# Kernel tuning notes

Measured on AMD Instinct MI355X. Metric: run time of the kernel, lower is better.

The kernel has to match this reference:

```python
import jax, jax.numpy as jnp
import numpy as np

N_IN, N_OUT, K, G = 128, 256, 3, 3  # G = grid intervals (setup hard-codes 3)
KNOT_LO, KNOT_HI = -1.0, 1.0


def make_grid(n, k, G, lo=KNOT_LO, hi=KNOT_HI):
    # Augmented knot vector: G+1 knots extended by k on each side -> G+2k+1 points
    h = (hi - lo) / G
    g = jnp.arange(-k, G + k + 1, dtype=jnp.float32) * h + lo
    return jnp.tile(g[None, :], (n, 1))  # (n, G+2k+1)


def get_spline_basis(x, grid, k):
    # Cox-de Boor recursion. x: (batch, n); grid: (n, G+2k+1)
    g = grid[None, :, :]          # (1, n, G+2k+1)
    xx = x[:, :, None]            # (batch, n, 1)
    # order-0 (indicator) basis: (batch, n, G+2k)
    basis = ((xx >= g[..., :-1]) & (xx < g[..., 1:])).astype(x.dtype)
    for kk in range(1, k + 1):
        left = (xx - g[..., : -(kk + 1)]) / (g[..., kk:-1] - g[..., : -(kk + 1)]) * basis[..., :-1]
        right = (g[..., kk + 1 :] - xx) / (g[..., kk + 1 :] - g[..., 1:-kk]) * basis[..., 1:]
        basis = left + right
    return basis  # (batch, n, G+k)


def setup_inputs() -> dict:
    key = jax.random.key(0)
    k1, k2 = jax.random.split(key)
    batch = 512
    n = N_IN * N_OUT
    x = jax.random.normal(k1, (batch, N_IN), dtype=jnp.float32)
    grid = make_grid(n, K, G)                                        # state (non-trainable)
    c_basis = 0.1 * jax.random.normal(k2, (n, G + K), dtype=jnp.float32)
    c_spl = jnp.ones((n,), dtype=jnp.float32)
    c_res = jnp.ones((n,), dtype=jnp.float32)
    return {"x": x, "grid": grid, "c_basis": c_basis, "c_spl": c_spl, "c_res": c_res}


def reference(x, grid, c_basis, c_spl, c_res):
    batch = x.shape[0]
    # Broadcast each input node to every output edge, out-major ordering:
    # einsum('ij,k->ikj', x, ones(n_out)).reshape(batch, n_in*n_out)
    x_ext = jnp.broadcast_to(x[:, None, :], (batch, N_OUT, N_IN)).reshape(batch, N_OUT * N_IN)
    # residual branch: swish, transposed to (n, batch)
    res = jax.nn.swish(x_ext).T
    # spline branch: (batch, n, G+K) basis combined with per-edge coeffs -> (n, batch)
    Bi = get_spline_basis(x_ext, grid, K)
    spl = jnp.einsum('ij,bij->ib', c_basis, Bi)
    y = c_spl[:, None] * spl + c_res[:, None] * res            # (n, batch)
    y = y.reshape(N_OUT, N_IN, batch).sum(axis=1) / N_IN       # (n_out, batch)
    return y.T                                                 # (batch, n_out)
```

## Files before the change

kernel.cpp:

```cpp
#include <hip/hip_runtime.h>
#include <hip/hip_bf16.h>


typedef short short8 __attribute__((ext_vector_type(8)));
typedef float f32x4 __attribute__((ext_vector_type(4)));

static __device__ inline unsigned short bf16_bits(float f) {
    union { __hip_bfloat16 h; unsigned short u; } cvt;
    cvt.h = __float2bfloat16(f);
    return cvt.u;
}

__global__ __launch_bounds__(256) void build_fw(
    const float* __restrict__ x,
    const float* __restrict__ grid,
    const float* __restrict__ c_basis,
    const float* __restrict__ c_spl,
    const float* __restrict__ c_res,
    unsigned short* __restrict__ F,
    unsigned short* __restrict__ W)
{
    const int tid = blockIdx.x * 256 + threadIdx.x;

    if (tid < 512 * 128) {
        float t[10];
#pragma unroll
        for (int m = 0; m < 10; ++m) t[m] = grid[m];

        const float xv = x[tid];

        float b0[9];
#pragma unroll
        for (int s = 0; s < 9; ++s)
            b0[s] = (xv >= t[s] && xv < t[s + 1]) ? 1.0f : 0.0f;
        float b1[8];
#pragma unroll
        for (int s = 0; s < 8; ++s)
            b1[s] = (xv - t[s]) / (t[s + 1] - t[s]) * b0[s]
                  + (t[s + 2] - xv) / (t[s + 2] - t[s + 1]) * b0[s + 1];
        float b2[7];
#pragma unroll
        for (int s = 0; s < 7; ++s)
            b2[s] = (xv - t[s]) / (t[s + 2] - t[s]) * b1[s]
                  + (t[s + 3] - xv) / (t[s + 3] - t[s + 1]) * b1[s + 1];
        float b3[6];
#pragma unroll
        for (int s = 0; s < 6; ++s)
            b3[s] = (xv - t[s]) / (t[s + 3] - t[s]) * b2[s]
                  + (t[s + 4] - xv) / (t[s + 4] - t[s + 1]) * b2[s + 1];

        const float sw = xv / (1.0f + expf(-xv));

        unsigned short* dst = F + tid * 7;
#pragma unroll
        for (int s = 0; s < 6; ++s) dst[s] = bf16_bits(b3[s]);
        dst[6] = bf16_bits(sw);
    } else if (tid < 512 * 128 + 32768) {
        const int j = tid - 512 * 128;
        unsigned short* dst = W + j * 7;
        const float spl = c_spl[j];
#pragma unroll
        for (int s = 0; s < 6; ++s) dst[s] = bf16_bits(spl * c_basis[j * 6 + s]);
        dst[6] = bf16_bits(c_res[j]);
    }
}

__global__ __launch_bounds__(64) void kan_gemm(
    const unsigned short* __restrict__ F,
    const unsigned short* __restrict__ W,
    float* __restrict__ out)
{
    const int bt   = blockIdx.x >> 4;
    const int ot   = blockIdx.x & 15;
    const int lane = threadIdx.x;
    const int r    = lane & 15;
    const int q    = lane >> 4;

    const unsigned short* fp = F + (bt * 16 + r) * 896 + q * 8;
    const unsigned short* wp = W + (ot * 16 + r) * 896 + q * 8;

    f32x4 acc = {0.0f, 0.0f, 0.0f, 0.0f};

#pragma unroll
    for (int k0 = 0; k0 < 896; k0 += 128) {
        short8 a0 = *(const short8*)(fp + k0);
        short8 a1 = *(const short8*)(fp + k0 + 32);
        short8 a2 = *(const short8*)(fp + k0 + 64);
        short8 a3 = *(const short8*)(fp + k0 + 96);
        short8 w0 = *(const short8*)(wp + k0);
        short8 w1 = *(const short8*)(wp + k0 + 32);
        short8 w2 = *(const short8*)(wp + k0 + 64);
        short8 w3 = *(const short8*)(wp + k0 + 96);
        acc = __builtin_amdgcn_mfma_f32_16x16x32_bf16(a0, w0, acc, 0, 0, 0);
        acc = __builtin_amdgcn_mfma_f32_16x16x32_bf16(a1, w1, acc, 0, 0, 0);
        acc = __builtin_amdgcn_mfma_f32_16x16x32_bf16(a2, w2, acc, 0, 0, 0);
        acc = __builtin_amdgcn_mfma_f32_16x16x32_bf16(a3, w3, acc, 0, 0, 0);
    }

    const float scale = 1.0f / 128.0f;
    const int orow = bt * 16 + q * 4;
    const int ocol = ot * 16 + r;
#pragma unroll
    for (int reg = 0; reg < 4; ++reg)
        out[(orow + reg) * 256 + ocol] = acc[reg] * scale;
}

extern "C" void kernel_launch(void* const* d_in, const int* in_sizes, int n_in,
                              void* d_out, int out_size, void* d_ws, size_t ws_size,
                              hipStream_t stream) {
    const float* x       = (const float*)d_in[0];
    const float* grid    = (const float*)d_in[1];
    const float* c_basis = (const float*)d_in[2];
    const float* c_spl   = (const float*)d_in[3];
    const float* c_res   = (const float*)d_in[4];
    float* out = (float*)d_out;

    unsigned short* F = (unsigned short*)d_ws;
    unsigned short* W = (unsigned short*)((char*)d_ws + 512 * 896 * 2);

    build_fw<<<384, 256, 0, stream>>>(x, grid, c_basis, c_spl, c_res, F, W);
    kan_gemm<<<512, 64, 0, stream>>>(F, W, out);
}
```

Before: 68.50 us.

## Fuse basis/weight construction and MFMA GEMM into one LDS-staged kernel

```diff
diff --git a/kernel.cpp b/kernel.cpp
--- a/kernel.cpp
+++ b/kernel.cpp
@@ -1,9 +1,13 @@
 #include <hip/hip_runtime.h>
 #include <hip/hip_bf16.h>
+#include <math.h>
 
 
 typedef short short8 __attribute__((ext_vector_type(8)));
 typedef float f32x4 __attribute__((ext_vector_type(4)));
+
+#define KDIM 896
+#define KPAD 904
 
 static __device__ inline unsigned short bf16_bits(float f) {
     union { __hip_bfloat16 h; unsigned short u; } cvt;
@@ -11,23 +15,32 @@
     return cvt.u;
 }
 
-__global__ __launch_bounds__(256) void build_fw(
+__global__ __launch_bounds__(128) void kan_fused(
     const float* __restrict__ x,
     const float* __restrict__ grid,
     const float* __restrict__ c_basis,
     const float* __restrict__ c_spl,
     const float* __restrict__ c_res,
-    unsigned short* __restrict__ F,
-    unsigned short* __restrict__ W)
+    float* __restrict__ out)
 {
-    const int tid = blockIdx.x * 256 + threadIdx.x;
+    extern __shared__ __align__(16) unsigned short smem[];
+    unsigned short* Fs = smem;
+    unsigned short* Ws = smem + 16 * KPAD;
 
-    if (tid < 512 * 128) {
-        float t[10];
+    const int bt  = blockIdx.x >> 3;
+    const int ot  = blockIdx.x & 7;
+    const int tid = threadIdx.x;
+
+    float t[10];
 #pragma unroll
-        for (int m = 0; m < 10; ++m) t[m] = grid[m];
+    for (int m = 0; m < 10; ++m) t[m] = grid[m];
+    const float ih1 = 1.0f / (t[1] - t[0]);
+    const float ih2 = 1.0f / (t[2] - t[0]);
+    const float ih3 = 1.0f / (t[3] - t[0]);
 
-        const float xv = x[tid];
+#pragma unroll 4
+    for (int p = 0; p < 16; ++p) {
+        const float xv = x[(bt * 16 + p) * 128 + tid];
 
         float b0[9];
 #pragma unroll
@@ -36,73 +49,63 @@
         float b1[8];
 #pragma unroll
         for (int s = 0; s < 8; ++s)
-            b1[s] = (xv - t[s]) / (t[s + 1] - t[s]) * b0[s]
-                  + (t[s + 2] - xv) / (t[s + 2] - t[s + 1]) * b0[s + 1];
+            b1[s] = (xv - t[s]) * ih1 * b0[s] + (t[s + 2] - xv) * ih1 * b0[s + 1];
         float b2[7];
 #pragma unroll
         for (int s = 0; s < 7; ++s)
-            b2[s] = (xv - t[s]) / (t[s + 2] - t[s]) * b1[s]
-                  + (t[s + 3] - xv) / (t[s + 3] - t[s + 1]) * b1[s + 1];
+            b2[s] = (xv - t[s]) * ih2 * b1[s] + (t[s + 3] - xv) * ih2 * b1[s + 1];
         float b3[6];
 #pragma unroll
         for (int s = 0; s < 6; ++s)
-            b3[s] = (xv - t[s]) / (t[s + 3] - t[s]) * b2[s]
-                  + (t[s + 4] - xv) / (t[s + 4] - t[s + 1]) * b2[s + 1];
+            b3[s] = (xv - t[s]) * ih3 * b2[s] + (t[s + 4] - xv) * ih3 * b2[s + 1];
 
         const float sw = xv / (1.0f + expf(-xv));
 
-        unsigned short* dst = F + tid * 7;
+        unsigned short* dst = Fs + p * KPAD + tid * 7;
 #pragma unroll
         for (int s = 0; s < 6; ++s) dst[s] = bf16_bits(b3[s]);
         dst[6] = bf16_bits(sw);
-    } else if (tid < 512 * 128 + 32768) {
-        const int j = tid - 512 * 128;
-        unsigned short* dst = W + j * 7;
+    }
+
+#pragma unroll 4
+    for (int p = 0; p < 32; ++p) {
+        const int j = (ot * 32 + p) * 128 + tid;
         const float spl = c_spl[j];
+        unsigned short* dst = Ws + p * KPAD + tid * 7;
 #pragma unroll
         for (int s = 0; s < 6; ++s) dst[s] = bf16_bits(spl * c_basis[j * 6 + s]);
         dst[6] = bf16_bits(c_res[j]);
     }
-}
 
-__global__ __launch_bounds__(64) void kan_gemm(
-    const unsigned short* __restrict__ F,
-    const unsigned short* __restrict__ W,
-    float* __restrict__ out)
-{
-    const int bt   = blockIdx.x >> 4;
-    const int ot   = blockIdx.x & 15;
-    const int lane = threadIdx.x;
+    __syncthreads();
+
+    const int lane = tid & 63;
+    const int w    = tid >> 6;
     const int r    = lane & 15;
     const int q    = lane >> 4;
 
-    const unsigned short* fp = F + (bt * 16 + r) * 896 + q * 8;
-    const unsigned short* wp = W + (ot * 16 + r) * 896 + q * 8;
+    const unsigned short* fa = Fs + r * KPAD + q * 8;
+    const unsigned short* wb = Ws + (w * 16 + r) * KPAD + q * 8;
 
-    f32x4 acc = {0.0f, 0.0f, 0.0f, 0.0f};
+    f32x4 acc0 = {0.f, 0.f, 0.f, 0.f};
+    f32x4 acc1 = {0.f, 0.f, 0.f, 0.f};
 
 #pragma unroll
-    for (int k0 = 0; k0 < 896; k0 += 128) {
-        short8 a0 = *(const short8*)(fp + k0);
-        short8 a1 = *(const short8*)(fp + k0 + 32);
-        short8 a2 = *(const short8*)(fp + k0 + 64);
-        short8 a3 = *(const short8*)(fp + k0 + 96);
-        short8 w0 = *(const short8*)(wp + k0);
-        short8 w1 = *(const short8*)(wp + k0 + 32);
-        short8 w2 = *(const short8*)(wp + k0 + 64);
-        short8 w3 = *(const short8*)(wp + k0 + 96);
-        acc = __builtin_amdgcn_mfma_f32_16x16x32_bf16(a0, w0, acc, 0, 0, 0);
-        acc = __builtin_amdgcn_mfma_f32_16x16x32_bf16(a1, w1, acc, 0, 0, 0);
-        acc = __builtin_amdgcn_mfma_f32_16x16x32_bf16(a2, w2, acc, 0, 0, 0);
-        acc = __builtin_amdgcn_mfma_f32_16x16x32_bf16(a3, w3, acc, 0, 0, 0);
+    for (int k0 = 0; k0 < KDIM; k0 += 64) {
+        short8 a0 = *(const short8*)(fa + k0);
+        short8 a1 = *(const short8*)(fa + k0 + 32);
+        short8 b0 = *(const short8*)(wb + k0);
+        short8 b1 = *(const short8*)(wb + k0 + 32);
+        acc0 = __builtin_amdgcn_mfma_f32_16x16x32_bf16(a0, b0, acc0, 0, 0, 0);
+        acc1 = __builtin_amdgcn_mfma_f32_16x16x32_bf16(a1, b1, acc1, 0, 0, 0);
     }
 
     const float scale = 1.0f / 128.0f;
-    const int orow = bt * 16 + q * 4;
-    const int ocol = ot * 16 + r;
+    const int orow0 = bt * 16 + q * 4;
+    const int ocol  = ot * 32 + w * 16 + r;
 #pragma unroll
-    for (int reg = 0; reg < 4; ++reg)
-        out[(orow + reg) * 256 + ocol] = acc[reg] * scale;
+    for (int e = 0; e < 4; ++e)
+        out[(orow0 + e) * 256 + ocol] = (acc0[e] + acc1[e]) * scale;
 }
 
 extern "C" void kernel_launch(void* const* d_in, const int* in_sizes, int n_in,
@@ -115,9 +118,6 @@
     const float* c_res   = (const float*)d_in[4];
     float* out = (float*)d_out;
 
-    unsigned short* F = (unsigned short*)d_ws;
-    unsigned short* W = (unsigned short*)((char*)d_ws + 512 * 896 * 2);
-
-    build_fw<<<384, 256, 0, stream>>>(x, grid, c_basis, c_spl, c_res, F, W);
-    kan_gemm<<<512, 64, 0, stream>>>(F, W, out);
+    const size_t smem_bytes = (16 + 32) * KPAD * sizeof(unsigned short);
+    kan_fused<<<256, 128, smem_bytes, stream>>>(x, grid, c_basis, c_spl, c_res, out);
 }
```

Measured after the change: 72.40 us. 1.06x slower.
